# Performance work log

Hardware: AMD Instinct MI355X
Metric: run time of the kernel (lower is better)

The kernel has to match this reference:

```python
import jax, jax.numpy as jnp
import numpy as np

B, L, D, K = 32, 128, 400, 40
RTOL, ATOL = 1e-4, 1e-6


def setup_inputs() -> dict:
    key = jax.random.key(0)
    ks = jax.random.split(key, 9)
    s = 0.3                      # input scale keeps exp(energy) in fp32 range
    u = 1.0 / np.sqrt(D)         # param scale
    input_h = jax.random.normal(ks[0], (B, L, D), jnp.float32) * s
    input_c = jax.random.normal(ks[1], (B, L, D), jnp.float32) * s
    W_d = jax.random.normal(ks[2], (K, D), jnp.float32) * u
    W_e = jax.random.normal(ks[3], (K, D), jnp.float32) * u
    U = jax.random.normal(ks[4], (K, D, D), jnp.float32) * u
    b = jax.random.normal(ks[5], (K,), jnp.float32) * 0.1
    heads = jax.random.randint(ks[6], (B, L), 0, L)
    pos = jnp.arange(L)[None, :]
    heads = jnp.where(heads == pos, (heads + 1) % L, heads)  # no self-loops (diag is -inf)
    arc_tags = jax.random.randint(ks[7], (B, L), 0, K)
    lengths = jax.random.randint(ks[8], (B,), L // 2, L + 1)
    mask = (jnp.arange(L)[None, :] < lengths[:, None]).astype(jnp.float32)
    return {"input_h": input_h, "input_c": input_c, "W_d": W_d, "W_e": W_e,
            "U": U, "b": b, "mask": mask, "heads": heads,
            "arc_tags": arc_tags, "lengths": lengths}


def reference(input_h, input_c, W_d, W_e, U, b, mask, heads, arc_tags, lengths):
    Bsz, Ln, _ = input_h.shape
    # --- BiAAttention: energy[b,k,head,child] ---
    bil = jnp.einsum('bhd,kde,bce->bkhc', input_h, U, input_c)
    sd = jnp.einsum('kd,bhd->bkh', W_d, input_h)[:, :, :, None]   # head bias
    se = jnp.einsum('kd,bcd->bkc', W_e, input_c)[:, :, None, :]   # child bias
    energy = bil + sd + se + b[None, :, None, None]
    energy = energy * mask[:, None, :, None] * mask[:, None, None, :]
    eye = jnp.eye(Ln, dtype=energy.dtype)
    energy = energy + jnp.where(eye > 0, -jnp.inf, 0.0)           # no self-arcs
    # --- Matrix-Tree partition function ---
    A = jnp.exp(energy) * mask[:, None, :, None] * mask[:, None, None, :]
    A = A.sum(axis=1)                                             # [B,L,L] over labels
    Dg = A.sum(axis=1) * (1.0 + RTOL) + ATOL                      # column (in-degree) sums
    Lap = eye * Dg[:, None, :] - A                                # Laplacian
    Sub = Lap[:, 1:, 1:]                                          # drop root row/col
    valid = jnp.arange(Ln - 1)[None, :] < (lengths - 1)[:, None]
    vm = valid[:, :, None] & valid[:, None, :]
    Sub = jnp.where(vm, Sub, jnp.eye(Ln - 1, dtype=Sub.dtype))    # identity-pad = logdet of [1:len,1:len]
    z = jnp.linalg.slogdet(Sub)[1]                                # [B]
    # --- gold-tree energy ---
    bi = jnp.arange(Bsz)[:, None]
    pos = jnp.arange(Ln)[None, :]
    te = energy[bi, arc_tags, heads, pos]                         # [B,L]
    tgt = te[:, 1:].sum(axis=1)
    return z - tgt
```

## Files before the change

### kernel.cpp

```cpp
#include <hip/hip_runtime.h>
#include <hip/hip_bf16.h>

#define BB 32
#define LL 128
#define DD 400
#define KK 40
#define EE 416
#define SDN 50
#define SEN 52

typedef __attribute__((ext_vector_type(8)))  short  bfrag;
typedef __attribute__((ext_vector_type(16))) float  ffrag;

static __device__ __forceinline__ short f2bf(float f) {
    union { float f; unsigned u; } v; v.f = f;
    unsigned r = (v.u + 0x7FFF + ((v.u >> 16) & 1)) >> 16;
    return (short)r;
}

#define MFMA32(a, b, c) __builtin_amdgcn_mfma_f32_32x32x16_bf16((a), (b), (c), 0, 0, 0)

static __device__ __forceinline__ void fzero(ffrag& f) {
#pragma unroll
    for (int r = 0; r < 16; ++r) f[r] = 0.f;
}

__global__ __launch_bounds__(256) void p_prep(
    const float* __restrict__ H, const float* __restrict__ C,
    const float* __restrict__ U,
    short* __restrict__ Hs, short* __restrict__ Cs, short* __restrict__ Us)
{
    int id = blockIdx.x * 256 + threadIdx.x;
    if (id < BB*SDN*LL) {
        int b = id / (SDN*LL); int r = id % (SDN*LL);
        int sd = r / LL; int h = r % LL;
        const float* src = H + ((size_t)(b*LL + h))*DD + sd*8;
        bfrag v;
#pragma unroll
        for (int j = 0; j < 8; ++j) v[j] = f2bf(src[j]);
        *(bfrag*)(Hs + (size_t)id*8) = v;
    } else if (id < BB*SDN*LL + BB*SEN*LL) {
        id -= BB*SDN*LL;
        int b = id / (SEN*LL); int r = id % (SEN*LL);
        int se = r / LL; int c = r % LL;
        bfrag v;
#pragma unroll
        for (int j = 0; j < 8; ++j) {
            int e = se*8 + j;
            v[j] = (e < DD) ? f2bf(C[((size_t)(b*LL + c))*DD + e]) : (short)0;
        }
        *(bfrag*)(Cs + (size_t)id*8) = v;
    } else {
        id -= BB*SDN*LL + BB*SEN*LL;
        int k = id / (SDN*EE); int r = id % (SDN*EE);
        int sd = r / EE; int e = r % EE;
        bfrag v;
#pragma unroll
        for (int j = 0; j < 8; ++j)
            v[j] = (e < DD) ? f2bf(U[((size_t)k*DD + sd*8 + j)*DD + e]) : (short)0;
        *(bfrag*)(Us + (size_t)id*8) = v;
    }
}

__global__ __launch_bounds__(256) void k_sdse(
    const float* __restrict__ H, const float* __restrict__ C,
    const float* __restrict__ Wd, const float* __restrict__ We,
    float* __restrict__ SD, float* __restrict__ SE)
{
    const int b   = blockIdx.x;
    const int rg  = blockIdx.y;
    const int srcC = blockIdx.z;
    const int t = threadIdx.x;

    __shared__ float Wl[KK*DD];
    {
        const float4* Wsrc = (const float4*)(srcC ? We : Wd);
        for (int i = t; i < KK*DD/4; i += 256) ((float4*)Wl)[i] = Wsrc[i];
    }
    __syncthreads();

    const int task = t >> 3;
    const int p    = t & 7;
    const int row  = rg*32 + task;
    const float* X = (srcC ? C : H) + ((size_t)(b*LL + row))*DD + p*50;

    float2 x[25];
#pragma unroll
    for (int i = 0; i < 25; ++i) x[i] = ((const float2*)X)[i];

    float* out = (srcC ? SE : SD) + (size_t)b*KK*LL + row;
    const float* Wb = Wl + p*50;

    for (int k = 0; k < KK; ++k) {
        const float2* wp = (const float2*)(Wb + k*DD);
        float s0 = 0.f, s1 = 0.f;
#pragma unroll
        for (int i = 0; i < 24; i += 2) {
            float2 w0 = wp[i], w1 = wp[i+1];
            s0 = fmaf(x[i].x,   w0.x, s0); s0 = fmaf(x[i].y,   w0.y, s0);
            s1 = fmaf(x[i+1].x, w1.x, s1); s1 = fmaf(x[i+1].y, w1.y, s1);
        }
        { float2 w0 = wp[24]; s0 = fmaf(x[24].x, w0.x, s0); s0 = fmaf(x[24].y, w0.y, s0); }
        float s = s0 + s1;
        s += __shfl_xor(s, 1); s += __shfl_xor(s, 2); s += __shfl_xor(s, 4);
        if (p == 0) out[k*LL] = s;
    }
}

static __device__ __forceinline__ void t_write(
    short* __restrict__ Ping, const ffrag& T, int et, int ht, int l31, int kh)
{
#pragma unroll
    for (int r = 0; r < 16; r += 2) {
        const int e_loc = 32*et + (r&3) + 8*(r>>2) + 4*kh;
        if (e_loc < DD) {
            unsigned lo = (unsigned short)f2bf(T[r]);
            unsigned hi = (unsigned short)f2bf(T[r+1]);
            *(unsigned*)(&Ping[((size_t)(e_loc>>3)*LL + 32*ht + l31)*8 + (e_loc&7)]) =
                lo | (hi << 16);
        }
    }
}

__global__ __launch_bounds__(1024) void k_mfma(
    const short* __restrict__ Hs, const short* __restrict__ Cs,
    const short* __restrict__ Us,
    const float* __restrict__ SD, const float* __restrict__ SE,
    const float* __restrict__ bvec, const float* __restrict__ mask,
    const int* __restrict__ heads, const int* __restrict__ tags,
    float* __restrict__ A8, float* __restrict__ tgt)
{
    const int b  = blockIdx.x;
    const int g  = blockIdx.y;
    const int t  = threadIdx.x;
    const int w  = t >> 6;
    const int l31 = t & 31;
    const int kh  = (t >> 5) & 1;

    __shared__ short Ping[SDN*LL*8];

    const size_t hsB = (size_t)b * SDN * LL;
    const size_t csB = (size_t)b * SEN * LL;

    const int ht2 = w >> 2;
    const int ct  = w & 3;
    const int hbase = 32*ht2 + 4*kh;
    const int c0 = 32*ct + l31;
    const float mc0 = mask[b*LL + c0];
    const int head0 = heads[b*LL + c0];
    const int tag0  = tags[b*LL + c0];
    unsigned vb = 0;
#pragma unroll
    for (int r = 0; r < 16; ++r) {
        const int hr = hbase + (r&3) + 8*(r>>2);
        if (mask[b*LL + hr] != 0.f && mc0 != 0.f && hr != c0) vb |= 1u << r;
    }

    ffrag E; fzero(E);

    for (int kk = 0; kk < 5; ++kk) {
        const int k = g + 8*kk;

        __syncthreads();

        {
            const uint4* src = (const uint4*)(Hs + hsB*8);
            uint4* dst = (uint4*)Ping;
            for (int i = t; i < SDN*LL*8*2/16; i += 1024) dst[i] = src[i];
        }
        __syncthreads();

        ffrag T0, T1, T2, T3;
        if (w < 13) {
            fzero(T0); fzero(T1); fzero(T2); fzero(T3);
            const int et = w;
            const short* up = Us + (((size_t)k*SDN + kh)*EE + 32*et + l31)*8;
            const short* hb = Ping + ((size_t)kh*LL + l31)*8;
#define UPF(j)    (*(const bfrag*)(up + (size_t)(j)*(2*EE*8)))
#define HPF(j,ht) (*(const bfrag*)(hb + ((size_t)(2*(j))*LL + 32*(ht))*8))
            bfrag a0 = UPF(0), a1 = UPF(1);
#pragma unroll 1
            for (int j = 0; j < 23; ++j) {
                bfrag an = UPF(j+2);
                bfrag b0 = HPF(j,0), b1 = HPF(j,1), b2 = HPF(j,2), b3 = HPF(j,3);
                T0 = MFMA32(a0, b0, T0); T1 = MFMA32(a0, b1, T1);
                T2 = MFMA32(a0, b2, T2); T3 = MFMA32(a0, b3, T3);
                a0 = a1; a1 = an;
            }
            {
                bfrag b0 = HPF(23,0), b1 = HPF(23,1), b2 = HPF(23,2), b3 = HPF(23,3);
                T0 = MFMA32(a0, b0, T0); T1 = MFMA32(a0, b1, T1);
                T2 = MFMA32(a0, b2, T2); T3 = MFMA32(a0, b3, T3);
                b0 = HPF(24,0); b1 = HPF(24,1); b2 = HPF(24,2); b3 = HPF(24,3);
                T0 = MFMA32(a1, b0, T0); T1 = MFMA32(a1, b1, T1);
                T2 = MFMA32(a1, b2, T2); T3 = MFMA32(a1, b3, T3);
            }
#undef UPF
#undef HPF
        }
        __syncthreads();

        if (w < 13) {
            t_write(Ping, T0, w, 0, l31, kh);
            t_write(Ping, T1, w, 1, l31, kh);
            t_write(Ping, T2, w, 2, l31, kh);
            t_write(Ping, T3, w, 3, l31, kh);
        }
        __syncthreads();

        ffrag S; fzero(S);
        const short* ta = Ping + ((size_t)kh*LL + 32*ht2 + l31)*8;
        const short* cp = Cs + (csB + (size_t)kh*LL + 32*ct + l31)*8;
#define TAF(j) (*(const bfrag*)(ta + (size_t)(2*(j))*(LL*8)))
#define CPF(j) (*(const bfrag*)(cp + (size_t)(2*(j))*(LL*8)))
        bfrag c0f = CPF(0), c1f = CPF(1), c2f = CPF(2);
        bfrag t0f = TAF(0), t1f = TAF(1);
#pragma unroll 1
        for (int j = 0; j < 22; ++j) {
            bfrag cn = CPF(j+3);
            bfrag tn = TAF(j+2);
            S = MFMA32(t0f, c0f, S);
            t0f = t1f; t1f = tn;
            c0f = c1f; c1f = c2f; c2f = cn;
        }
        S = MFMA32(t0f, c0f, S);
        S = MFMA32(t1f, c1f, S);
        S = MFMA32(TAF(24), c2f, S);
#undef TAF
#undef CPF

        const float bk = bvec[k];
        const float* SDb = SD + ((size_t)b*KK + k)*LL;
        const float sev = SE[((size_t)b*KK + k)*LL + c0];
#pragma unroll
        for (int r = 0; r < 16; ++r) {
            const int hr = hbase + (r&3) + 8*(r>>2);
            const float ev = S[r] + SDb[hr] + sev + bk;
            if ((vb >> r) & 1) {
                E[r] += __expf(ev);
                if (c0 >= 1 && tag0 == k && head0 == hr) atomicAdd(&tgt[b], ev);
            }
        }
    }

    float* Ab = A8 + ((size_t)(g*BB + b))*LL*LL;
#pragma unroll
    for (int r = 0; r < 16; ++r) {
        const int hr = hbase + (r&3) + 8*(r>>2);
        Ab[hr*LL + c0] = E[r];
    }
}

__global__ __launch_bounds__(256) void k_logdet(
    const float* __restrict__ A8, const int* __restrict__ lengths,
    const float* __restrict__ tgt, float* __restrict__ out)
{
    const int b = blockIdx.x;
    const int t = threadIdx.x;
    const int rg = t >> 4;
    const int cg = t & 15;

    __shared__ float As[LL*LL];
    __shared__ float Dg[128];
    __shared__ float Lbuf[128];
    __shared__ float Ubuf[128];
    __shared__ float red[256];

    const float4* A4 = (const float4*)A8;
    for (int f4 = t; f4 < 4096; f4 += 256) {
        float4 s = make_float4(0.f, 0.f, 0.f, 0.f);
#pragma unroll
        for (int g = 0; g < 8; ++g) {
            float4 v = A4[((size_t)(g*BB + b))*4096 + f4];
            s.x += v.x; s.y += v.y; s.z += v.z; s.w += v.w;
        }
        ((float4*)As)[f4] = s;
    }
    __syncthreads();

    if (t < 128) {
        float s = 0.f;
        for (int hr = 0; hr < LL; ++hr) s += As[hr*LL + t];
        Dg[t] = s * (1.0f + 1e-4f) + 1e-6f;
    }
    __syncthreads();

    const int n1 = lengths[b] - 1;
    float m[8][8];
#pragma unroll
    for (int r = 0; r < 8; ++r) {
        const int i = 8*rg + r;
#pragma unroll
        for (int c = 0; c < 8; ++c) {
            const int j = 8*cg + c;
            float v;
            if (i < n1 && j < n1)
                v = ((i == j) ? Dg[i+1] : 0.f) - As[(i+1)*LL + (j+1)];
            else
                v = (i == j) ? 1.f : 0.f;
            m[r][c] = v;
        }
    }
    __syncthreads();

    for (int j = 0; j < 127; ++j) {
        const int jg = j >> 3, jl = j & 7;
        if (cg == jg) {
#pragma unroll
            for (int c = 0; c < 8; ++c) {
                if (c == jl) {
#pragma unroll
                    for (int r = 0; r < 8; ++r) Lbuf[8*rg + r] = m[r][c];
                }
            }
        }
        if (rg == jg) {
#pragma unroll
            for (int r = 0; r < 8; ++r) {
                if (r == jl) {
#pragma unroll
                    for (int c = 0; c < 8; ++c) Ubuf[8*cg + c] = m[r][c];
                }
            }
        }
        __syncthreads();

        const float piv = Lbuf[j];
        if (t == j) Dg[j] = piv;
        const float rp = 1.0f / piv;
        float lr[8], ur[8];
#pragma unroll
        for (int r = 0; r < 8; ++r) lr[r] = Lbuf[8*rg + r] * rp;
#pragma unroll
        for (int c = 0; c < 8; ++c) ur[c] = Ubuf[8*cg + c];
#pragma unroll
        for (int r = 0; r < 8; ++r)
#pragma unroll
            for (int c = 0; c < 8; ++c)
                m[r][c] = fmaf(-lr[r], ur[c], m[r][c]);
        __syncthreads();
    }

    float lsum = 0.f;
    if (t < 127) lsum = logf(Dg[t]);
    red[t] = lsum;
    __syncthreads();
    for (int off = 128; off >= 1; off >>= 1) {
        if (t < off) red[t] += red[t + off];
        __syncthreads();
    }
    if (t == 0) out[b] = red[0] - tgt[b];
}

extern "C" void kernel_launch(void* const* d_in, const int* in_sizes, int n_in,
                              void* d_out, int out_size, void* d_ws, size_t ws_size,
                              hipStream_t stream) {
    const float* H    = (const float*)d_in[0];
    const float* C    = (const float*)d_in[1];
    const float* Wd   = (const float*)d_in[2];
    const float* We   = (const float*)d_in[3];
    const float* U    = (const float*)d_in[4];
    const float* bv   = (const float*)d_in[5];
    const float* mask = (const float*)d_in[6];
    const int* heads  = (const int*)d_in[7];
    const int* tags   = (const int*)d_in[8];
    const int* lens   = (const int*)d_in[9];
    float* out = (float*)d_out;

    char* p = (char*)d_ws;
    float* A8  = (float*)p;                 p += (size_t)8*BB*LL*LL*4;
    float* tgt = (float*)p;                 p += 32*4;
    float* SDp = (float*)p;                 p += (size_t)BB*KK*LL*4;
    float* SEp = (float*)p;                 p += (size_t)BB*KK*LL*4;
    short* Hsp = (short*)p;                 p += (size_t)BB*SDN*LL*8*2;
    short* Csp = (short*)p;                 p += (size_t)BB*SEN*LL*8*2;
    short* Usp = (short*)p;                 p += (size_t)KK*SDN*EE*8*2;

    hipMemsetAsync(tgt, 0, 32*4, stream);

    p_prep<<<dim3(4882), 256, 0, stream>>>(H, C, U, Hsp, Csp, Usp);
    k_sdse<<<dim3(BB, 4, 2), 256, 0, stream>>>(H, C, Wd, We, SDp, SEp);
    k_mfma<<<dim3(BB, 8), 1024, 0, stream>>>(Hsp, Csp, Usp, SDp, SEp, bv, mask,
                                             heads, tags, A8, tgt);
    k_logdet<<<dim3(BB), 256, 0, stream>>>(A8, lens, tgt, out);
}
```

Before: 344.9 us.

## Fold tgt zeroing into sdse kernel, unroll MFMA loops, split Dg reduction

Removes the separate hipMemsetAsync by zeroing tgt inside k_sdse. k_mfma's two MFMA loops are fully unrolled instead of software-pipelined by hand, the second loop gets two independent accumulators to shorten dependency chains, and the kernel gets a min-blocks launch bound. The column-sum reduction in k_logdet now uses all 256 threads in two halves. Full unrolling and the launch bound may raise register pressure or change the schedule in unpredictable ways.

```diff
diff --git a/kernel.cpp b/kernel.cpp
--- a/kernel.cpp
+++ b/kernel.cpp
@@ -65,12 +65,14 @@
 __global__ __launch_bounds__(256) void k_sdse(
     const float* __restrict__ H, const float* __restrict__ C,
     const float* __restrict__ Wd, const float* __restrict__ We,
-    float* __restrict__ SD, float* __restrict__ SE)
+    float* __restrict__ SD, float* __restrict__ SE, float* __restrict__ tgt)
 {
     const int b   = blockIdx.x;
     const int rg  = blockIdx.y;
     const int srcC = blockIdx.z;
     const int t = threadIdx.x;
+
+    if (rg == 0 && srcC == 0 && t == 0) tgt[b] = 0.f;
 
     __shared__ float Wl[KK*DD];
     {
@@ -122,7 +124,7 @@
     }
 }
 
-__global__ __launch_bounds__(1024) void k_mfma(
+__global__ __launch_bounds__(1024, 4) void k_mfma(
     const short* __restrict__ Hs, const short* __restrict__ Cs,
     const short* __restrict__ Us,
     const float* __restrict__ SD, const float* __restrict__ SE,
@@ -178,22 +180,13 @@
             const short* hb = Ping + ((size_t)kh*LL + l31)*8;
 #define UPF(j)    (*(const bfrag*)(up + (size_t)(j)*(2*EE*8)))
 #define HPF(j,ht) (*(const bfrag*)(hb + ((size_t)(2*(j))*LL + 32*(ht))*8))
-            bfrag a0 = UPF(0), a1 = UPF(1);
-#pragma unroll 1
-            for (int j = 0; j < 23; ++j) {
-                bfrag an = UPF(j+2);
-                bfrag b0 = HPF(j,0), b1 = HPF(j,1), b2 = HPF(j,2), b3 = HPF(j,3);
-                T0 = MFMA32(a0, b0, T0); T1 = MFMA32(a0, b1, T1);
-                T2 = MFMA32(a0, b2, T2); T3 = MFMA32(a0, b3, T3);
-                a0 = a1; a1 = an;
-            }
-            {
-                bfrag b0 = HPF(23,0), b1 = HPF(23,1), b2 = HPF(23,2), b3 = HPF(23,3);
-                T0 = MFMA32(a0, b0, T0); T1 = MFMA32(a0, b1, T1);
-                T2 = MFMA32(a0, b2, T2); T3 = MFMA32(a0, b3, T3);
-                b0 = HPF(24,0); b1 = HPF(24,1); b2 = HPF(24,2); b3 = HPF(24,3);
-                T0 = MFMA32(a1, b0, T0); T1 = MFMA32(a1, b1, T1);
-                T2 = MFMA32(a1, b2, T2); T3 = MFMA32(a1, b3, T3);
+#pragma unroll
+            for (int j = 0; j < 25; ++j) {
+                const bfrag av = UPF(j);
+                T0 = MFMA32(av, HPF(j,0), T0);
+                T1 = MFMA32(av, HPF(j,1), T1);
+                T2 = MFMA32(av, HPF(j,2), T2);
+                T3 = MFMA32(av, HPF(j,3), T3);
             }
 #undef UPF
 #undef HPF
@@ -208,24 +201,17 @@
         }
         __syncthreads();
 
-        ffrag S; fzero(S);
+        ffrag Sa, Sb; fzero(Sa); fzero(Sb);
         const short* ta = Ping + ((size_t)kh*LL + 32*ht2 + l31)*8;
         const short* cp = Cs + (csB + (size_t)kh*LL + 32*ct + l31)*8;
 #define TAF(j) (*(const bfrag*)(ta + (size_t)(2*(j))*(LL*8)))
 #define CPF(j) (*(const bfrag*)(cp + (size_t)(2*(j))*(LL*8)))
-        bfrag c0f = CPF(0), c1f = CPF(1), c2f = CPF(2);
-        bfrag t0f = TAF(0), t1f = TAF(1);
-#pragma unroll 1
-        for (int j = 0; j < 22; ++j) {
-            bfrag cn = CPF(j+3);
-            bfrag tn = TAF(j+2);
-            S = MFMA32(t0f, c0f, S);
-            t0f = t1f; t1f = tn;
-            c0f = c1f; c1f = c2f; c2f = cn;
-        }
-        S = MFMA32(t0f, c0f, S);
-        S = MFMA32(t1f, c1f, S);
-        S = MFMA32(TAF(24), c2f, S);
+#pragma unroll
+        for (int j = 0; j < 24; j += 2) {
+            Sa = MFMA32(TAF(j),   CPF(j),   Sa);
+            Sb = MFMA32(TAF(j+1), CPF(j+1), Sb);
+        }
+        Sa = MFMA32(TAF(24), CPF(24), Sa);
 #undef TAF
 #undef CPF
 
@@ -235,7 +221,7 @@
 #pragma unroll
         for (int r = 0; r < 16; ++r) {
             const int hr = hbase + (r&3) + 8*(r>>2);
-            const float ev = S[r] + SDb[hr] + sev + bk;
+            const float ev = Sa[r] + Sb[r] + SDb[hr] + sev + bk;
             if ((vb >> r) & 1) {
                 E[r] += __expf(ev);
                 if (c0 >= 1 && tag0 == k && head0 == hr) atomicAdd(&tgt[b], ev);
@@ -278,11 +264,14 @@
     }
     __syncthreads();
 
-    if (t < 128) {
+    {
+        const int col = t & 127, half = t >> 7;
         float s = 0.f;
-        for (int hr = 0; hr < LL; ++hr) s += As[hr*LL + t];
-        Dg[t] = s * (1.0f + 1e-4f) + 1e-6f;
-    }
+        for (int hr = half*64; hr < half*64 + 64; ++hr) s += As[hr*LL + col];
+        red[t] = s;
+    }
+    __syncthreads();
+    if (t < 128) Dg[t] = (red[t] + red[t+128]) * (1.0f + 1e-4f) + 1e-6f;
     __syncthreads();
 
     const int n1 = lengths[b] - 1;
@@ -376,10 +365,8 @@
     short* Csp = (short*)p;                 p += (size_t)BB*SEN*LL*8*2;
     short* Usp = (short*)p;                 p += (size_t)KK*SDN*EE*8*2;
 
-    hipMemsetAsync(tgt, 0, 32*4, stream);
-
     p_prep<<<dim3(4882), 256, 0, stream>>>(H, C, U, Hsp, Csp, Usp);
-    k_sdse<<<dim3(BB, 4, 2), 256, 0, stream>>>(H, C, Wd, We, SDp, SEp);
+    k_sdse<<<dim3(BB, 4, 2), 256, 0, stream>>>(H, C, Wd, We, SDp, SEp, tgt);
     k_mfma<<<dim3(BB, 8), 1024, 0, stream>>>(Hsp, Csp, Usp, SDp, SEp, bv, mask,
                                              heads, tags, A8, tgt);
     k_logdet<<<dim3(BB), 256, 0, stream>>>(A8, lens, tgt, out);
```

Result: slower. 989.9 us (+187.0%).

## Software-pipeline LDS loads in MFMA loop, widen stores, drop memset, split degree sum

Applied to the files above, without the earlier changes.

Several small changes. The first GEMM loop now prefetches the next step's H fragments from shared memory and interleaves loads with MFMAs, to hide LDS latency. The bf16 transpose writes are widened from 32-bit to 64-bit stores. The memset of tgt is removed; k_sdse zeroes tgt instead, saving one launch. The column-degree sum in k_logdet is split over all 256 threads, with a final reduction step. Extra live fragment registers could raise register pressure in the 1024-thread MFMA kernel.

```diff
diff --git a/kernel.cpp b/kernel.cpp
--- a/kernel.cpp
+++ b/kernel.cpp
@@ -65,13 +65,15 @@
 __global__ __launch_bounds__(256) void k_sdse(
     const float* __restrict__ H, const float* __restrict__ C,
     const float* __restrict__ Wd, const float* __restrict__ We,
-    float* __restrict__ SD, float* __restrict__ SE)
+    float* __restrict__ SD, float* __restrict__ SE, float* __restrict__ tgt)
 {
     const int b   = blockIdx.x;
     const int rg  = blockIdx.y;
     const int srcC = blockIdx.z;
     const int t = threadIdx.x;
 
+    if (rg == 0 && srcC == 0 && t == 0) tgt[b] = 0.f;
+
     __shared__ float Wl[KK*DD];
     {
         const float4* Wsrc = (const float4*)(srcC ? We : Wd);
@@ -111,13 +113,16 @@
     short* __restrict__ Ping, const ffrag& T, int et, int ht, int l31, int kh)
 {
 #pragma unroll
-    for (int r = 0; r < 16; r += 2) {
-        const int e_loc = 32*et + (r&3) + 8*(r>>2) + 4*kh;
-        if (e_loc < DD) {
-            unsigned lo = (unsigned short)f2bf(T[r]);
-            unsigned hi = (unsigned short)f2bf(T[r+1]);
-            *(unsigned*)(&Ping[((size_t)(e_loc>>3)*LL + 32*ht + l31)*8 + (e_loc&7)]) =
-                lo | (hi << 16);
+    for (int q = 0; q < 4; ++q) {
+        const int e_base = 32*et + 8*q + 4*kh;
+        if (e_base < DD) {
+            const int r = 4*q;
+            uint2 v;
+            v.x = (unsigned)(unsigned short)f2bf(T[r])
+                | ((unsigned)(unsigned short)f2bf(T[r+1]) << 16);
+            v.y = (unsigned)(unsigned short)f2bf(T[r+2])
+                | ((unsigned)(unsigned short)f2bf(T[r+3]) << 16);
+            *(uint2*)(&Ping[((size_t)(e_base>>3)*LL + 32*ht + l31)*8 + (e_base&7)]) = v;
         }
     }
 }
@@ -179,21 +184,33 @@
 #define UPF(j)    (*(const bfrag*)(up + (size_t)(j)*(2*EE*8)))
 #define HPF(j,ht) (*(const bfrag*)(hb + ((size_t)(2*(j))*LL + 32*(ht))*8))
             bfrag a0 = UPF(0), a1 = UPF(1);
+            bfrag hA = HPF(0,0), hB = HPF(0,1);
 #pragma unroll 1
             for (int j = 0; j < 23; ++j) {
-                bfrag an = UPF(j+2);
-                bfrag b0 = HPF(j,0), b1 = HPF(j,1), b2 = HPF(j,2), b3 = HPF(j,3);
-                T0 = MFMA32(a0, b0, T0); T1 = MFMA32(a0, b1, T1);
-                T2 = MFMA32(a0, b2, T2); T3 = MFMA32(a0, b3, T3);
-                a0 = a1; a1 = an;
+                bfrag hC = HPF(j,2), hD = HPF(j,3);
+                T0 = MFMA32(a0, hA, T0);
+                T1 = MFMA32(a0, hB, T1);
+                bfrag hA2 = HPF(j+1,0), hB2 = HPF(j+1,1);
+                bfrag an  = UPF(j+2);
+                T2 = MFMA32(a0, hC, T2);
+                T3 = MFMA32(a0, hD, T3);
+                a0 = a1; a1 = an; hA = hA2; hB = hB2;
             }
             {
-                bfrag b0 = HPF(23,0), b1 = HPF(23,1), b2 = HPF(23,2), b3 = HPF(23,3);
-                T0 = MFMA32(a0, b0, T0); T1 = MFMA32(a0, b1, T1);
-                T2 = MFMA32(a0, b2, T2); T3 = MFMA32(a0, b3, T3);
-                b0 = HPF(24,0); b1 = HPF(24,1); b2 = HPF(24,2); b3 = HPF(24,3);
-                T0 = MFMA32(a1, b0, T0); T1 = MFMA32(a1, b1, T1);
-                T2 = MFMA32(a1, b2, T2); T3 = MFMA32(a1, b3, T3);
+                bfrag hC = HPF(23,2), hD = HPF(23,3);
+                T0 = MFMA32(a0, hA, T0);
+                T1 = MFMA32(a0, hB, T1);
+                bfrag hA2 = HPF(24,0), hB2 = HPF(24,1);
+                T2 = MFMA32(a0, hC, T2);
+                T3 = MFMA32(a0, hD, T3);
+                a0 = a1; hA = hA2; hB = hB2;
+            }
+            {
+                bfrag hC = HPF(24,2), hD = HPF(24,3);
+                T0 = MFMA32(a0, hA, T0);
+                T1 = MFMA32(a0, hB, T1);
+                T2 = MFMA32(a0, hC, T2);
+                T3 = MFMA32(a0, hD, T3);
             }
 #undef UPF
 #undef HPF
@@ -278,11 +295,14 @@
     }
     __syncthreads();
 
-    if (t < 128) {
+    {
+        const int col = t & 127, half = t >> 7;
         float s = 0.f;
-        for (int hr = 0; hr < LL; ++hr) s += As[hr*LL + t];
-        Dg[t] = s * (1.0f + 1e-4f) + 1e-6f;
-    }
+        for (int hr = half*64; hr < half*64 + 64; ++hr) s += As[hr*LL + col];
+        red[t] = s;
+    }
+    __syncthreads();
+    if (t < 128) Dg[t] = (red[t] + red[t+128]) * (1.0f + 1e-4f) + 1e-6f;
     __syncthreads();
 
     const int n1 = lengths[b] - 1;
@@ -376,10 +396,8 @@
     short* Csp = (short*)p;                 p += (size_t)BB*SEN*LL*8*2;
     short* Usp = (short*)p;                 p += (size_t)KK*SDN*EE*8*2;
 
-    hipMemsetAsync(tgt, 0, 32*4, stream);
-
     p_prep<<<dim3(4882), 256, 0, stream>>>(H, C, U, Hsp, Csp, Usp);
-    k_sdse<<<dim3(BB, 4, 2), 256, 0, stream>>>(H, C, Wd, We, SDp, SEp);
+    k_sdse<<<dim3(BB, 4, 2), 256, 0, stream>>>(H, C, Wd, We, SDp, SEp, tgt);
     k_mfma<<<dim3(BB, 8), 1024, 0, stream>>>(Hsp, Csp, Usp, SDp, SEp, bv, mask,
                                              heads, tags, A8, tgt);
     k_logdet<<<dim3(BB), 256, 0, stream>>>(A8, lens, tgt, out);
```

Result: faster. 337.7 us (-2.1%).
